# Kernel tuning notes

Hardware: AMD Instinct MI355X
Metric: run time of the kernel (lower is better)

## Reference

```python
import jax, jax.numpy as jnp
import numpy as np

LAMBDA_ENERGY = 0.1   # CONFIG['lambda_energy']
EPS = 1e-6            # CONFIG['eps']
TEMP = 1.0


def setup_inputs() -> dict:
    key = jax.random.key(0)
    k0, k1, k2, k3, k4 = jax.random.split(key, 5)
    B, S, D, N = 8, 4096, 512, 1024
    z_real = jax.random.normal(k0, (B, S, D), dtype=jnp.float32)
    z_imag = jax.random.normal(k1, (B, S, D), dtype=jnp.float32)
    # prev symbol distribution: a proper simplex distribution over symbols
    prev_sym_dist = jax.nn.softmax(jax.random.normal(k2, (B, S, N), dtype=jnp.float32), axis=-1)
    codebook = jax.random.normal(k3, (N, 2 * D), dtype=jnp.float32) * 0.2
    adjacency_energy = jax.random.normal(k4, (N, N), dtype=jnp.float32)
    return {"z_real": z_real, "z_imag": z_imag, "prev_sym_dist": prev_sym_dist,
            "codebook": codebook, "adjacency_energy": adjacency_energy}


def reference(z_real, z_imag, prev_sym_dist, codebook, adjacency_energy):
    D = z_real.shape[-1]
    z_flat = jnp.concatenate([z_real, z_imag], axis=-1)  # [B,S,2D]

    # squared-distance to codebook entries, normalized by feature dim
    d_content = (jnp.sum(z_flat * z_flat, axis=-1, keepdims=True)
                 + jnp.sum(codebook * codebook, axis=-1)
                 - 2.0 * jnp.einsum('bsd,nd->bsn', z_flat, codebook)) / z_flat.shape[-1]

    # ComplexityModulator (eval mode): running_var buffer == 1.0
    mag = jnp.sqrt(z_real * z_real + z_imag * z_imag)  # |z|
    batch_var = jnp.var(mag, ddof=1)                   # torch .var() is unbiased
    modulation = jax.nn.softplus(batch_var / (1.0 + EPS))

    # graph-bias gating
    graph_bias = jnp.einsum('bsn,nm->bsm', prev_sym_dist, adjacency_energy)
    d_total = d_content - (LAMBDA_ENERGY * modulation) * jax.nn.sigmoid(graph_bias)

    # eval path: soft_one_hot = softmax(logits / temp)
    probs = jax.nn.softmax(-d_total / TEMP, axis=-1)   # [B,S,N]
    z_q_flat = jnp.einsum('bsn,nd->bsd', probs, codebook)  # [B,S,2D]

    energy = jnp.mean(d_total)
    return z_q_flat[..., :D], z_q_flat[..., D:], energy
```

## Files before the change

kernel.cpp:

```cpp
#include <hip/hip_runtime.h>

typedef float    floatx4 __attribute__((ext_vector_type(4)));
typedef short    short8  __attribute__((ext_vector_type(8)));
typedef _Float16 h4      __attribute__((ext_vector_type(4)));

#define NROWS 32768
#define KD    1024
#define DD    512

__device__ __forceinline__ unsigned pk_bf16(unsigned hi_bits, unsigned lo_bits) {
    return __builtin_amdgcn_perm(hi_bits, lo_bits, 0x07060302u);
}

__device__ __forceinline__ void gload_lds16(const void* g, void* l) {
    __builtin_amdgcn_global_load_lds((__attribute__((address_space(1))) void*)(void*)g,
                                     (__attribute__((address_space(3))) void*)l,
                                     16, 0, 0);
}

__global__ void k_row(const float* __restrict__ zr, const float* __restrict__ zi,
                      unsigned short* __restrict__ zb,
                      float* __restrict__ zz, float* __restrict__ mgp) {
    int r = blockIdx.x, t = threadIdx.x;
    const float2* a2 = (const float2*)(zr + (size_t)r * DD);
    const float2* b2 = (const float2*)(zi + (size_t)r * DD);
    float2 a = a2[t], b = b2[t];
    unsigned* zrow = (unsigned*)(zb + (size_t)r * KD);
    zrow[t]       = pk_bf16(__float_as_uint(a.y), __float_as_uint(a.x));
    zrow[256 + t] = pk_bf16(__float_as_uint(b.y), __float_as_uint(b.x));
    float m0 = a.x * a.x + b.x * b.x;
    float m1 = a.y * a.y + b.y * b.y;
    float sm2 = m0 + m1;
    float smg = sqrtf(m0) + sqrtf(m1);
    for (int o = 32; o > 0; o >>= 1) { sm2 += __shfl_down(sm2, o); smg += __shfl_down(smg, o); }
    __shared__ float r2[4], rg[4];
    int wv = t >> 6, ln = t & 63;
    if (ln == 0) { r2[wv] = sm2; rg[wv] = smg; }
    __syncthreads();
    if (t == 0) {
        zz[r]  = r2[0] + r2[1] + r2[2] + r2[3];
        mgp[r] = rg[0] + rg[1] + rg[2] + rg[3];
    }
}

__global__ void k_prev(const float* __restrict__ p, unsigned short* __restrict__ pb) {
    size_t i = ((size_t)blockIdx.x * 256 + threadIdx.x) * 8;
    const uint4* g = (const uint4*)(p + i);
    uint4 u0 = g[0], u1 = g[1];
    uint4 o;
    o.x = pk_bf16(u0.y, u0.x); o.y = pk_bf16(u0.w, u0.z);
    o.z = pk_bf16(u1.y, u1.x); o.w = pk_bf16(u1.w, u1.z);
    *(uint4*)(pb + i) = o;
}

__global__ void k_cb(const float* __restrict__ cb, unsigned short* __restrict__ cb_bf,
                     float* __restrict__ cc) {
    int n = blockIdx.x, t = threadIdx.x;
    const float4* src = (const float4*)(cb + (size_t)n * KD);
    float4 v = src[t];
    float s = v.x * v.x + v.y * v.y + v.z * v.z + v.w * v.w;
    unsigned d0 = pk_bf16(__float_as_uint(v.y), __float_as_uint(v.x));
    unsigned d1 = pk_bf16(__float_as_uint(v.w), __float_as_uint(v.z));
    *(uint2*)(cb_bf + (size_t)n * KD + t * 4) = make_uint2(d0, d1);
    for (int o = 32; o > 0; o >>= 1) s += __shfl_down(s, o);
    __shared__ float rd[4];
    int wv = t >> 6, ln = t & 63;
    if (ln == 0) rd[wv] = s;
    __syncthreads();
    if (t == 0) cc[n] = rd[0] + rd[1] + rd[2] + rd[3];
}

__global__ void k_tr(const float* __restrict__ src, unsigned short* __restrict__ dst) {
    __shared__ float tile[32][33];
    int bx = blockIdx.x * 32, by = blockIdx.y * 32;
    int tx = threadIdx.x, ty = threadIdx.y;
    for (int r = ty; r < 32; r += 8)
        tile[r][tx] = src[(size_t)(by + r) * 1024 + bx + tx];
    __syncthreads();
    for (int r = ty; r < 32; r += 8)
        dst[(size_t)(bx + r) * 1024 + by + tx] =
            (unsigned short)(__float_as_uint(tile[tx][r]) >> 16);
}

__global__ void k_scalar(const float* __restrict__ zz, const float* __restrict__ mgp,
                         double* __restrict__ sums, float* __restrict__ lam) {
    int t = threadIdx.x;
    double s2 = 0.0, sg = 0.0;
    for (int i = t; i < NROWS; i += 1024) { s2 += (double)zz[i]; sg += (double)mgp[i]; }
    __shared__ double l2[1024], lg[1024];
    l2[t] = s2; lg[t] = sg; __syncthreads();
    for (int s = 512; s > 0; s >>= 1) {
        if (t < s) { l2[t] += l2[t + s]; lg[t] += lg[t + s]; }
        __syncthreads();
    }
    if (t == 0) {
        double M = 16777216.0;
        double var = (l2[0] - lg[0] * lg[0] / M) / (M - 1.0);
        double x = var / (1.0 + 1e-6);
        double mod = log1p(exp(x));
        lam[0] = (float)(0.1 * mod);
        sums[1] = l2[0];
    }
}

__device__ __forceinline__ void gemm_mainloop(
    const unsigned short* __restrict__ Ap, const unsigned short* __restrict__ Bp,
    int row0, int col0, int wv, int ln,
    unsigned short* As, unsigned short* Bs, floatx4 (&acc)[4][4]) {
    int wr = (wv >> 1) * 64, wc = (wv & 1) * 64;
    size_t sa[4], sbo[4];
    int dst[4];
    #pragma unroll
    for (int j = 0; j < 4; ++j) {
        int g = j * 256 + wv * 64 + ln;
        int r = g >> 3, s0 = g & 7;
        size_t co = (size_t)((s0 ^ (r & 7)) << 3);
        sa[j]  = (size_t)(row0 + r) * KD + co;
        sbo[j] = (size_t)(col0 + r) * KD + co;
        dst[j] = (j * 256 + wv * 64) * 8;
    }
    for (int kb = 0; kb < KD; kb += 64) {
        #pragma unroll
        for (int j = 0; j < 4; ++j) gload_lds16(Ap + sa[j] + kb, &As[dst[j]]);
        #pragma unroll
        for (int j = 0; j < 4; ++j) gload_lds16(Bp + sbo[j] + kb, &Bs[dst[j]]);
        __syncthreads();
        #pragma unroll
        for (int kk = 0; kk < 2; ++kk) {
            int sbi = kk * 4 + (ln >> 4);
            short8 af[4], bf[4];
            #pragma unroll
            for (int i = 0; i < 4; ++i) {
                int r = wr + i * 16 + (ln & 15);
                af[i] = *(const short8*)&As[r * 64 + ((sbi ^ (r & 7)) << 3)];
            }
            #pragma unroll
            for (int j = 0; j < 4; ++j) {
                int r = wc + j * 16 + (ln & 15);
                bf[j] = *(const short8*)&Bs[r * 64 + ((sbi ^ (r & 7)) << 3)];
            }
            #pragma unroll
            for (int mi = 0; mi < 4; ++mi)
                #pragma unroll
                for (int ni = 0; ni < 4; ++ni)
                    acc[mi][ni] = __builtin_amdgcn_mfma_f32_16x16x32_bf16(af[mi], bf[ni], acc[mi][ni], 0, 0, 0);
        }
        __syncthreads();
    }
}

__global__ __launch_bounds__(256, 4)
void k_gemm1(const unsigned short* __restrict__ zb,
             const unsigned short* __restrict__ cb_bf,
             const float* __restrict__ cc, _Float16* __restrict__ s_out) {
    __shared__ unsigned short As[128 * 64], Bs[128 * 64];
    int tid = threadIdx.x, bid = blockIdx.x;
    int wg = (bid & 7) * 256 + (bid >> 3);
    int rt = wg >> 3, ct = wg & 7;
    int row0 = rt * 128, col0 = ct * 128;
    int wv = tid >> 6, ln = tid & 63;
    floatx4 acc[4][4];
    #pragma unroll
    for (int i = 0; i < 4; ++i)
        #pragma unroll
        for (int j = 0; j < 4; ++j) { floatx4 z4 = {0.f, 0.f, 0.f, 0.f}; acc[i][j] = z4; }
    gemm_mainloop(zb, cb_bf, row0, col0, wv, ln, As, Bs, acc);

    int wr = (wv >> 1) * 64, wc = (wv & 1) * 64;
    for (int mi = 0; mi < 4; ++mi) {
        int rbase = row0 + wr + mi * 16 + (ln >> 4) * 4;
        for (int ni = 0; ni < 4; ++ni) {
            int col = col0 + wc + ni * 16 + (ln & 15);
            float ccol = cc[col];
            for (int r2 = 0; r2 < 4; ++r2) {
                float sv = (ccol - 2.f * acc[mi][ni][r2]) * (1.0f / 1024.0f);
                s_out[(size_t)(rbase + r2) * KD + col] = (_Float16)sv;
            }
        }
    }
}

__global__ __launch_bounds__(256, 4)
void k_gemm2(const unsigned short* __restrict__ pb,
             const unsigned short* __restrict__ adjT_bf,
             const float* __restrict__ lam_p,
             _Float16* __restrict__ s_io, double* __restrict__ e_acc) {
    __shared__ unsigned short As[128 * 64], Bs[128 * 64];
    int tid = threadIdx.x, bid = blockIdx.x;
    int wg = (bid & 7) * 256 + (bid >> 3);
    int rt = wg >> 3, ct = wg & 7;
    int row0 = rt * 128, col0 = ct * 128;
    int wv = tid >> 6, ln = tid & 63;
    floatx4 acc[4][4];
    #pragma unroll
    for (int i = 0; i < 4; ++i)
        #pragma unroll
        for (int j = 0; j < 4; ++j) { floatx4 z4 = {0.f, 0.f, 0.f, 0.f}; acc[i][j] = z4; }
    gemm_mainloop(pb, adjT_bf, row0, col0, wv, ln, As, Bs, acc);

    int wr = (wv >> 1) * 64, wc = (wv & 1) * 64;
    float lam = *lam_p;
    float esum = 0.f;
    for (int mi = 0; mi < 4; ++mi) {
        int rbase = row0 + wr + mi * 16 + (ln >> 4) * 4;
        for (int ni = 0; ni < 4; ++ni) {
            int col = col0 + wc + ni * 16 + (ln & 15);
            for (int r2 = 0; r2 < 4; ++r2) {
                size_t idx = (size_t)(rbase + r2) * KD + col;
                float sv = (float)s_io[idx] - lam / (1.f + __expf(-acc[mi][ni][r2]));
                esum += sv;
                s_io[idx] = (_Float16)sv;
            }
        }
    }
    for (int o = 32; o > 0; o >>= 1) esum += __shfl_down(esum, o);
    if (ln == 0) atomicAdd(e_acc, (double)esum);
}

__global__ void k_softmax(_Float16* __restrict__ sp) {
    int row = blockIdx.x, t = threadIdx.x;
    int wv = t >> 6, ln = t & 63;
    _Float16* srow = sp + (size_t)row * KD;
    h4 v = *(const h4*)(srow + t * 4);
    float x0 = -(float)v.x, x1 = -(float)v.y, x2 = -(float)v.z, x3 = -(float)v.w;
    float mx = fmaxf(fmaxf(x0, x1), fmaxf(x2, x3));
    for (int o = 1; o < 64; o <<= 1) mx = fmaxf(mx, __shfl_xor(mx, o));
    __shared__ float redm[4];
    if (ln == 0) redm[wv] = mx;
    __syncthreads();
    mx = fmaxf(fmaxf(redm[0], redm[1]), fmaxf(redm[2], redm[3]));
    float e0 = __expf(x0 - mx), e1 = __expf(x1 - mx), e2 = __expf(x2 - mx), e3 = __expf(x3 - mx);
    float ss = e0 + e1 + e2 + e3;
    for (int o = 1; o < 64; o <<= 1) ss += __shfl_xor(ss, o);
    __shared__ float reds[4];
    if (ln == 0) reds[wv] = ss;
    __syncthreads();
    ss = reds[0] + reds[1] + reds[2] + reds[3];
    float inv = 1.f / ss;
    unsigned p0 = __float_as_uint(e0 * inv), p1 = __float_as_uint(e1 * inv);
    unsigned p2 = __float_as_uint(e2 * inv), p3 = __float_as_uint(e3 * inv);
    *(uint2*)((unsigned short*)srow + t * 4) = make_uint2(pk_bf16(p1, p0), pk_bf16(p3, p2));
}

__global__ __launch_bounds__(256, 4)
void k_gemm3(const unsigned short* __restrict__ probs,
             const unsigned short* __restrict__ cbT_bf,
             float* __restrict__ outR, float* __restrict__ outI) {
    __shared__ unsigned short As[128 * 64], Bs[128 * 64];
    int tid = threadIdx.x, bid = blockIdx.x;
    int wg = (bid & 7) * 256 + (bid >> 3);
    int rt = wg >> 3, ct = wg & 7;
    int row0 = rt * 128, col0 = ct * 128;
    int wv = tid >> 6, ln = tid & 63;
    floatx4 acc[4][4];
    #pragma unroll
    for (int i = 0; i < 4; ++i)
        #pragma unroll
        for (int j = 0; j < 4; ++j) { floatx4 z4 = {0.f, 0.f, 0.f, 0.f}; acc[i][j] = z4; }
    gemm_mainloop(probs, cbT_bf, row0, col0, wv, ln, As, Bs, acc);

    int wr = (wv >> 1) * 64, wc = (wv & 1) * 64;
    for (int mi = 0; mi < 4; ++mi) {
        int rbase = row0 + wr + mi * 16 + (ln >> 4) * 4;
        for (int ni = 0; ni < 4; ++ni) {
            int col = col0 + wc + ni * 16 + (ln & 15);
            for (int r2 = 0; r2 < 4; ++r2) {
                float v = acc[mi][ni][r2];
                size_t row = (size_t)(rbase + r2);
                if (col < DD) outR[row * DD + col] = v;
                else          outI[row * DD + (col - DD)] = v;
            }
        }
    }
}

__global__ void k_final(const double* __restrict__ sums, float* __restrict__ outE) {
    outE[0] = (float)((sums[0] + sums[1]) / 33554432.0);
}

extern "C" void kernel_launch(void* const* d_in, const int* in_sizes, int n_in,
                              void* d_out, int out_size, void* d_ws, size_t ws_size,
                              hipStream_t stream) {
    const float* zr   = (const float*)d_in[0];
    const float* zi   = (const float*)d_in[1];
    const float* prev = (const float*)d_in[2];
    const float* cb   = (const float*)d_in[3];
    const float* adj  = (const float*)d_in[4];
    float* out  = (float*)d_out;
    float* outR = out;
    float* outI = out + (size_t)16777216;
    float* outE = out + (size_t)33554432;

    unsigned short* zb = (unsigned short*)d_out;
    unsigned short* pb = (unsigned short*)d_out + (size_t)33554432;

    char* ws = (char*)d_ws;
    double* sums          = (double*)ws;
    float*  lam           = (float*)(ws + 16);
    float*  zz            = (float*)(ws + 256);
    float*  mgp           = (float*)(ws + 131328);
    float*  cc            = (float*)(ws + 262400);
    unsigned short* cb_bf = (unsigned short*)(ws + 266496);
    unsigned short* adjT  = (unsigned short*)(ws + 2363648);
    unsigned short* cbT   = (unsigned short*)(ws + 4460800);
    _Float16*       sbuf  = (_Float16*)(ws + 6557952);

    hipMemsetAsync(d_ws, 0, 32, stream);
    k_row<<<32768, 256, 0, stream>>>(zr, zi, zb, zz, mgp);
    k_prev<<<16384, 256, 0, stream>>>(prev, pb);
    k_cb<<<1024, 256, 0, stream>>>(cb, cb_bf, cc);
    k_tr<<<dim3(32, 32), dim3(32, 8), 0, stream>>>(adj, adjT);
    k_tr<<<dim3(32, 32), dim3(32, 8), 0, stream>>>(cb, cbT);
    k_scalar<<<1, 1024, 0, stream>>>(zz, mgp, sums, lam);
    k_gemm1<<<2048, 256, 0, stream>>>(zb, cb_bf, cc, sbuf);
    k_gemm2<<<2048, 256, 0, stream>>>(pb, adjT, lam, sbuf, sums);
    k_softmax<<<32768, 256, 0, stream>>>(sbuf);
    k_gemm3<<<2048, 256, 0, stream>>>((const unsigned short*)sbuf, cbT, outR, outI);
    k_final<<<1, 1, 0, stream>>>(sums, outE);
}
```

Before: 646.1 us.

## Rewrite GEMM mainloop as 256x256 tiles with double-buffered LDS pipeline

Replaces the 128x128 single-buffered GEMM mainloop with 256x256 tiles on 512-thread (8-wave) blocks. Global-to-LDS loads are double-buffered and interleaved with MFMA phases using explicit vmcnt waits, barriers, sched_barrier and setprio. The goal is to raise arithmetic intensity and to hide load latency behind compute in all three GEMMs. In exchange it uses 128 KB of LDS per block and twice the accumulator registers, which lowers occupancy and depends on hand-tuned wait counts being correct.

```diff
diff --git a/kernel.cpp b/kernel.cpp
--- a/kernel.cpp
+++ b/kernel.cpp
@@ -103,74 +103,124 @@
     }
 }
 
-__device__ __forceinline__ void gemm_mainloop(
-    const unsigned short* __restrict__ Ap, const unsigned short* __restrict__ Bp,
-    int row0, int col0, int wv, int ln,
-    unsigned short* As, unsigned short* Bs, floatx4 (&acc)[4][4]) {
-    int wr = (wv >> 1) * 64, wc = (wv & 1) * 64;
-    size_t sa[4], sbo[4];
-    int dst[4];
+#define STG_A(c,h,kb) do { \
+    gload_lds16(Ap + offA[(h)*2+0] + (kb), &As[(c)*16384 + (h)*8192 + wv*512]); \
+    gload_lds16(Ap + offA[(h)*2+1] + (kb), &As[(c)*16384 + (h)*8192 + 4096 + wv*512]); } while(0)
+#define STG_B(c,h,kb) do { \
+    gload_lds16(Bp + offB[(h)*2+0] + (kb), &Bs[(c)*16384 + (h)*8192 + wv*512]); \
+    gload_lds16(Bp + offB[(h)*2+1] + (kb), &Bs[(c)*16384 + (h)*8192 + 4096 + wv*512]); } while(0)
+#define WAIT4 do { asm volatile("s_waitcnt vmcnt(4)" ::: "memory"); \
+                   __builtin_amdgcn_sched_barrier(0); } while(0)
+#define WAIT0 do { asm volatile("s_waitcnt vmcnt(0)" ::: "memory"); \
+                   __builtin_amdgcn_sched_barrier(0); } while(0)
+#define PHASE(c, q, STMT, WCNT)                                                     \
+  do {                                                                              \
+    if ((q) == 0) {                                                                 \
+      _Pragma("unroll") for (int ni = 0; ni < 4; ++ni)                              \
+      _Pragma("unroll") for (int kk = 0; kk < 2; ++kk) {                            \
+        int row = brow + ni * 16;                                                   \
+        int sl = (kk * 4 + sl_hi) ^ sx;                                             \
+        bfrag[ni][kk] = *(const short8*)&Bs[(c) * 16384 + row * 64 + (sl << 3)];    \
+      }                                                                             \
+    }                                                                               \
+    short8 afr[2][2];                                                               \
+    _Pragma("unroll") for (int im = 0; im < 2; ++im)                                \
+    _Pragma("unroll") for (int kk = 0; kk < 2; ++kk) {                              \
+      int row = arow + ((q) * 2 + im) * 16;                                         \
+      int sl = (kk * 4 + sl_hi) ^ sx;                                               \
+      afr[im][kk] = *(const short8*)&As[(c) * 16384 + row * 64 + (sl << 3)];        \
+    }                                                                               \
+    STMT;                                                                           \
+    __builtin_amdgcn_s_barrier();                                                   \
+    asm volatile("s_waitcnt lgkmcnt(0)" ::: "memory");                              \
+    __builtin_amdgcn_sched_barrier(0);                                              \
+    __builtin_amdgcn_s_setprio(1);                                                  \
+    _Pragma("unroll") for (int kk = 0; kk < 2; ++kk)                                \
+    _Pragma("unroll") for (int im = 0; im < 2; ++im)                                \
+    _Pragma("unroll") for (int ni = 0; ni < 4; ++ni)                                \
+      acc[(q) * 2 + im][ni] = __builtin_amdgcn_mfma_f32_16x16x32_bf16(              \
+          afr[im][kk], bfrag[ni][kk], acc[(q) * 2 + im][ni], 0, 0, 0);              \
+    __builtin_amdgcn_s_setprio(0);                                                  \
+    WCNT;                                                                           \
+    __builtin_amdgcn_s_barrier();                                                   \
+  } while (0)
+
+__device__ __forceinline__ void mm256(const unsigned short* __restrict__ Ap,
+                                      const unsigned short* __restrict__ Bp,
+                                      int row0g, int col0g,
+                                      unsigned short* As, unsigned short* Bs,
+                                      floatx4 (&acc)[8][4]) {
+    const int tid = threadIdx.x;
+    const int wv = tid >> 6, ln = tid & 63;
+    const int wm = wv >> 2, wn = wv & 3;
+    const int r0 = tid >> 3, s0 = tid & 7;
+
+    unsigned offA[4], offB[4];
     #pragma unroll
-    for (int j = 0; j < 4; ++j) {
-        int g = j * 256 + wv * 64 + ln;
-        int r = g >> 3, s0 = g & 7;
-        size_t co = (size_t)((s0 ^ (r & 7)) << 3);
-        sa[j]  = (size_t)(row0 + r) * KD + co;
-        sbo[j] = (size_t)(col0 + r) * KD + co;
-        dst[j] = (j * 256 + wv * 64) * 8;
-    }
-    for (int kb = 0; kb < KD; kb += 64) {
-        #pragma unroll
-        for (int j = 0; j < 4; ++j) gload_lds16(Ap + sa[j] + kb, &As[dst[j]]);
-        #pragma unroll
-        for (int j = 0; j < 4; ++j) gload_lds16(Bp + sbo[j] + kb, &Bs[dst[j]]);
-        __syncthreads();
-        #pragma unroll
-        for (int kk = 0; kk < 2; ++kk) {
-            int sbi = kk * 4 + (ln >> 4);
-            short8 af[4], bf[4];
-            #pragma unroll
-            for (int i = 0; i < 4; ++i) {
-                int r = wr + i * 16 + (ln & 15);
-                af[i] = *(const short8*)&As[r * 64 + ((sbi ^ (r & 7)) << 3)];
-            }
-            #pragma unroll
-            for (int j = 0; j < 4; ++j) {
-                int r = wc + j * 16 + (ln & 15);
-                bf[j] = *(const short8*)&Bs[r * 64 + ((sbi ^ (r & 7)) << 3)];
-            }
-            #pragma unroll
-            for (int mi = 0; mi < 4; ++mi)
-                #pragma unroll
-                for (int ni = 0; ni < 4; ++ni)
-                    acc[mi][ni] = __builtin_amdgcn_mfma_f32_16x16x32_bf16(af[mi], bf[ni], acc[mi][ni], 0, 0, 0);
-        }
-        __syncthreads();
-    }
-}
-
-__global__ __launch_bounds__(256, 4)
+    for (int u = 0; u < 4; ++u) {
+        int r = u * 64 + r0;
+        unsigned co = (unsigned)((s0 ^ (r & 7)) << 3);
+        offA[u] = (unsigned)(row0g + r) * KD + co;
+        offB[u] = (unsigned)(col0g + r) * KD + co;
+    }
+    const int arow = wm * 128 + (ln & 15);
+    const int brow = wn * 64 + (ln & 15);
+    const int sl_hi = ln >> 4;
+    const int sx = ln & 7;
+    short8 bfrag[4][2];
+
+    STG_A(0, 0, 0); STG_A(0, 1, 0); STG_B(0, 0, 0); STG_B(0, 1, 0);
+    STG_B(1, 0, 64); STG_B(1, 1, 64);
+    WAIT4;
+    __builtin_amdgcn_s_barrier();
+
+    for (int i = 0; i < 7; ++i) {
+        const int kb = i * 128;
+        PHASE(0, 0, { STG_A(1, 0, kb + 64); STG_A(1, 1, kb + 64); }, );
+        PHASE(0, 1, { STG_B(0, 0, kb + 128); }, );
+        PHASE(0, 2, { STG_B(0, 1, kb + 128); }, );
+        PHASE(0, 3, { }, WAIT4);
+        PHASE(1, 0, { STG_A(0, 0, kb + 128); STG_A(0, 1, kb + 128); }, );
+        PHASE(1, 1, { STG_B(1, 0, kb + 192); }, );
+        PHASE(1, 2, { STG_B(1, 1, kb + 192); }, );
+        PHASE(1, 3, { }, WAIT4);
+    }
+    {
+        const int kb = 7 * 128;
+        PHASE(0, 0, { STG_A(1, 0, kb + 64); STG_A(1, 1, kb + 64); }, );
+        PHASE(0, 1, { }, );
+        PHASE(0, 2, { }, );
+        PHASE(0, 3, { }, WAIT0);
+        PHASE(1, 0, { }, );
+        PHASE(1, 1, { }, );
+        PHASE(1, 2, { }, );
+        PHASE(1, 3, { }, );
+    }
+}
+
+__global__ __launch_bounds__(512, 2)
 void k_gemm1(const unsigned short* __restrict__ zb,
              const unsigned short* __restrict__ cb_bf,
              const float* __restrict__ cc, _Float16* __restrict__ s_out) {
-    __shared__ unsigned short As[128 * 64], Bs[128 * 64];
+    __shared__ unsigned short As[32768], Bs[32768];
     int tid = threadIdx.x, bid = blockIdx.x;
-    int wg = (bid & 7) * 256 + (bid >> 3);
-    int rt = wg >> 3, ct = wg & 7;
-    int row0 = rt * 128, col0 = ct * 128;
+    int wg = (bid & 7) * 64 + (bid >> 3);
+    int rt = wg >> 2, ct = wg & 3;
+    int row0 = rt * 256, col0 = ct * 256;
     int wv = tid >> 6, ln = tid & 63;
-    floatx4 acc[4][4];
+    int wm = wv >> 2, wn = wv & 3;
+    floatx4 acc[8][4];
     #pragma unroll
-    for (int i = 0; i < 4; ++i)
+    for (int i = 0; i < 8; ++i)
         #pragma unroll
         for (int j = 0; j < 4; ++j) { floatx4 z4 = {0.f, 0.f, 0.f, 0.f}; acc[i][j] = z4; }
-    gemm_mainloop(zb, cb_bf, row0, col0, wv, ln, As, Bs, acc);
-
-    int wr = (wv >> 1) * 64, wc = (wv & 1) * 64;
-    for (int mi = 0; mi < 4; ++mi) {
-        int rbase = row0 + wr + mi * 16 + (ln >> 4) * 4;
+    mm256(zb, cb_bf, row0, col0, As, Bs, acc);
+
+    int wrow = row0 + wm * 128, wcol = col0 + wn * 64;
+    for (int mi = 0; mi < 8; ++mi) {
+        int rbase = wrow + mi * 16 + (ln >> 4) * 4;
         for (int ni = 0; ni < 4; ++ni) {
-            int col = col0 + wc + ni * 16 + (ln & 15);
+            int col = wcol + ni * 16 + (ln & 15);
             float ccol = cc[col];
             for (int r2 = 0; r2 < 4; ++r2) {
                 float sv = (ccol - 2.f * acc[mi][ni][r2]) * (1.0f / 1024.0f);
@@ -180,31 +230,32 @@
     }
 }
 
-__global__ __launch_bounds__(256, 4)
+__global__ __launch_bounds__(512, 2)
 void k_gemm2(const unsigned short* __restrict__ pb,
              const unsigned short* __restrict__ adjT_bf,
              const float* __restrict__ lam_p,
              _Float16* __restrict__ s_io, double* __restrict__ e_acc) {
-    __shared__ unsigned short As[128 * 64], Bs[128 * 64];
+    __shared__ unsigned short As[32768], Bs[32768];
     int tid = threadIdx.x, bid = blockIdx.x;
-    int wg = (bid & 7) * 256 + (bid >> 3);
-    int rt = wg >> 3, ct = wg & 7;
-    int row0 = rt * 128, col0 = ct * 128;
+    int wg = (bid & 7) * 64 + (bid >> 3);
+    int rt = wg >> 2, ct = wg & 3;
+    int row0 = rt * 256, col0 = ct * 256;
     int wv = tid >> 6, ln = tid & 63;
-    floatx4 acc[4][4];
+    int wm = wv >> 2, wn = wv & 3;
+    floatx4 acc[8][4];
     #pragma unroll
-    for (int i = 0; i < 4; ++i)
+    for (int i = 0; i < 8; ++i)
         #pragma unroll
         for (int j = 0; j < 4; ++j) { floatx4 z4 = {0.f, 0.f, 0.f, 0.f}; acc[i][j] = z4; }
-    gemm_mainloop(pb, adjT_bf, row0, col0, wv, ln, As, Bs, acc);
-
-    int wr = (wv >> 1) * 64, wc = (wv & 1) * 64;
+    mm256(pb, adjT_bf, row0, col0, As, Bs, acc);
+
+    int wrow = row0 + wm * 128, wcol = col0 + wn * 64;
     float lam = *lam_p;
     float esum = 0.f;
-    for (int mi = 0; mi < 4; ++mi) {
-        int rbase = row0 + wr + mi * 16 + (ln >> 4) * 4;
+    for (int mi = 0; mi < 8; ++mi) {
+        int rbase = wrow + mi * 16 + (ln >> 4) * 4;
         for (int ni = 0; ni < 4; ++ni) {
-            int col = col0 + wc + ni * 16 + (ln & 15);
+            int col = wcol + ni * 16 + (ln & 15);
             for (int r2 = 0; r2 < 4; ++r2) {
                 size_t idx = (size_t)(rbase + r2) * KD + col;
                 float sv = (float)s_io[idx] - lam / (1.f + __expf(-acc[mi][ni][r2]));
@@ -242,28 +293,29 @@
     *(uint2*)((unsigned short*)srow + t * 4) = make_uint2(pk_bf16(p1, p0), pk_bf16(p3, p2));
 }
 
-__global__ __launch_bounds__(256, 4)
+__global__ __launch_bounds__(512, 2)
 void k_gemm3(const unsigned short* __restrict__ probs,
              const unsigned short* __restrict__ cbT_bf,
              float* __restrict__ outR, float* __restrict__ outI) {
-    __shared__ unsigned short As[128 * 64], Bs[128 * 64];
+    __shared__ unsigned short As[32768], Bs[32768];
     int tid = threadIdx.x, bid = blockIdx.x;
-    int wg = (bid & 7) * 256 + (bid >> 3);
-    int rt = wg >> 3, ct = wg & 7;
-    int row0 = rt * 128, col0 = ct * 128;
+    int wg = (bid & 7) * 64 + (bid >> 3);
+    int rt = wg >> 2, ct = wg & 3;
+    int row0 = rt * 256, col0 = ct * 256;
     int wv = tid >> 6, ln = tid & 63;
-    floatx4 acc[4][4];
+    int wm = wv >> 2, wn = wv & 3;
+    floatx4 acc[8][4];
     #pragma unroll
-    for (int i = 0; i < 4; ++i)
+    for (int i = 0; i < 8; ++i)
         #pragma unroll
         for (int j = 0; j < 4; ++j) { floatx4 z4 = {0.f, 0.f, 0.f, 0.f}; acc[i][j] = z4; }
-    gemm_mainloop(probs, cbT_bf, row0, col0, wv, ln, As, Bs, acc);
-
-    int wr = (wv >> 1) * 64, wc = (wv & 1) * 64;
-    for (int mi = 0; mi < 4; ++mi) {
-        int rbase = row0 + wr + mi * 16 + (ln >> 4) * 4;
+    mm256(probs, cbT_bf, row0, col0, As, Bs, acc);
+
+    int wrow = row0 + wm * 128, wcol = col0 + wn * 64;
+    for (int mi = 0; mi < 8; ++mi) {
+        int rbase = wrow + mi * 16 + (ln >> 4) * 4;
         for (int ni = 0; ni < 4; ++ni) {
-            int col = col0 + wc + ni * 16 + (ln & 15);
+            int col = wcol + ni * 16 + (ln & 15);
             for (int r2 = 0; r2 < 4; ++r2) {
                 float v = acc[mi][ni][r2];
                 size_t row = (size_t)(rbase + r2);
@@ -312,9 +364,9 @@
     k_tr<<<dim3(32, 32), dim3(32, 8), 0, stream>>>(adj, adjT);
     k_tr<<<dim3(32, 32), dim3(32, 8), 0, stream>>>(cb, cbT);
     k_scalar<<<1, 1024, 0, stream>>>(zz, mgp, sums, lam);
-    k_gemm1<<<2048, 256, 0, stream>>>(zb, cb_bf, cc, sbuf);
-    k_gemm2<<<2048, 256, 0, stream>>>(pb, adjT, lam, sbuf, sums);
+    k_gemm1<<<512, 512, 0, stream>>>(zb, cb_bf, cc, sbuf);
+    k_gemm2<<<512, 512, 0, stream>>>(pb, adjT, lam, sbuf, sums);
     k_softmax<<<32768, 256, 0, stream>>>(sbuf);
-    k_gemm3<<<2048, 256, 0, stream>>>((const unsigned short*)sbuf, cbT, outR, outI);
+    k_gemm3<<<512, 512, 0, stream>>>((const unsigned short*)sbuf, cbT, outR, outI);
     k_final<<<1, 1, 0, stream>>>(sums, outE);
 }
```

Result: slower. 673.5 us (+4.2%).
